# Optimization experiments

Hardware: AMD Instinct MI355X
Metric: run time of the kernel (lower is better)

The kernel has to match this reference:

```python
import jax, jax.numpy as jnp
import numpy as np

HIDDEN = 1024
H2 = HIDDEN // 2
LAYERS = 2
NUM_CONDS = 4


def _lstm_dir(x, Wih, Whh, b, reverse):
    # x: (B, T, I); Wih: (4*H2, I); Whh: (4*H2, H2); b: (4*H2,)
    B = x.shape[0]
    h2 = Whh.shape[1]
    pre = jnp.einsum('bti,gi->btg', x, Wih) + b  # precompute input contribution
    pre = jnp.swapaxes(pre, 0, 1)  # (T, B, 4*H2)
    if reverse:
        pre = pre[::-1]

    def step(carry, g_in):
        h, c = carry
        g = g_in + h @ Whh.T
        i, f, gg, o = jnp.split(g, 4, axis=-1)
        c = jax.nn.sigmoid(f) * c + jax.nn.sigmoid(i) * jnp.tanh(gg)
        h = jax.nn.sigmoid(o) * jnp.tanh(c)
        return (h, c), h

    init = (jnp.zeros((B, h2), x.dtype), jnp.zeros((B, h2), x.dtype))
    _, hs = jax.lax.scan(step, init, pre)
    if reverse:
        hs = hs[::-1]
    return jnp.swapaxes(hs, 0, 1)  # (B, T, H2)


def _bilstm(x, Wih, Whh, b):
    # Wih: (L, 2, 4*H2, I) — all layers share input width since embed_dim == hidden_dim
    out = x
    for l in range(Wih.shape[0]):
        fwd = _lstm_dir(out, Wih[l, 0], Whh[l, 0], b[l, 0], False)
        bwd = _lstm_dir(out, Wih[l, 1], Whh[l, 1], b[l, 1], True)
        out = jnp.concatenate([fwd, bwd], axis=-1)
    return out


def setup_inputs() -> dict:
    key = jax.random.key(0)
    ks = jax.random.split(key, 24)
    s = 0.02
    G = 4 * H2
    inp = {
        'question_embedding': jax.random.normal(ks[0], (32, 128, 1024), jnp.float32),
        'packed_column_embedding': jax.random.normal(ks[1], (640, 8, 1024), jnp.float32),
        'gold_num': jax.random.randint(ks[2], (32,), 0, 5),
        'gold_cols': jax.random.randint(ks[3], (32, 4), 0, 20),
        'gold_ops': jax.random.randint(ks[4], (32, 4), 0, 4),
        'num_columns': 20,
        'q_Wih': jax.random.normal(ks[5], (LAYERS, 2, G, 1024), jnp.float32) * s,
        'q_Whh': jax.random.normal(ks[6], (LAYERS, 2, G, H2), jnp.float32) * s,
        'q_b': jax.random.normal(ks[7], (LAYERS, 2, G), jnp.float32) * s,
        'c_Wih': jax.random.normal(ks[8], (LAYERS, 2, G, 1024), jnp.float32) * s,
        'c_Whh': jax.random.normal(ks[9], (LAYERS, 2, G, H2), jnp.float32) * s,
        'c_b': jax.random.normal(ks[10], (LAYERS, 2, G), jnp.float32) * s,
        'col_attn_w': jax.random.normal(ks[11], (1, HIDDEN), jnp.float32) * s,
        'col_attn_b': jnp.zeros((1,), jnp.float32),
        'ob_attn_W': jax.random.normal(ks[12], (HIDDEN, HIDDEN), jnp.float32) * s,
        'ob_attn_b': jnp.zeros((HIDDEN,), jnp.float32),
        'ob_col_W': jax.random.normal(ks[13], (HIDDEN, HIDDEN), jnp.float32) * s,
        'ob_col_b': jnp.zeros((HIDDEN,), jnp.float32),
        'q_proj_W': jax.random.normal(ks[14], (HIDDEN, HIDDEN), jnp.float32) * s,
        'q_proj_b': jnp.zeros((HIDDEN,), jnp.float32),
        'out1_W': jax.random.normal(ks[15], (HIDDEN, 3 * HIDDEN), jnp.float32) * s,
        'out1_b': jnp.zeros((HIDDEN,), jnp.float32),
        'out2_W': jax.random.normal(ks[16], (2, HIDDEN), jnp.float32) * s,
        'out2_b': jnp.zeros((2,), jnp.float32),
    }
    return inp


def _forward(question_embedding, packed_column_embedding, gold_num, gold_cols,
             num_columns, q_Wih, q_Whh, q_b, c_Wih, c_Whh, c_b,
             col_attn_w, col_attn_b, ob_attn_W, ob_attn_b, ob_col_W, ob_col_b,
             q_proj_W, q_proj_b, out1_W, out1_b, out2_W, out2_b):
    dt = question_embedding.dtype
    bs, Tq, _ = question_embedding.shape
    # compute_mask: nonzero token positions
    q_mask = (jnp.abs(question_embedding).sum(-1) != 0).astype(dt)  # (B, Tq)
    c_mask = (jnp.abs(packed_column_embedding).sum(-1) != 0).astype(dt)  # (P, Tc)

    q_enc = _bilstm(question_embedding, q_Wih, q_Whh, q_b)  # (B, Tq, H)
    c_enc = _bilstm(packed_column_embedding, c_Wih, c_Whh, c_b)  # (P, Tc, H)

    # attention-pool each column name: make_weight = masked softmax over tokens
    logits = jnp.einsum('pth,oh->pt', c_enc, col_attn_w) + col_attn_b[0]
    logits = jnp.where(c_mask > 0, logits, -jnp.inf)
    w = jax.nn.softmax(logits, axis=-1)
    col_pooled = jnp.einsum('pt,pth->ph', w, c_enc)  # (P, H)
    column_hidden = col_pooled.reshape(bs, num_columns, HIDDEN)  # (B, NC, H)

    # get_observed_column_hidden (torch.no_grad): gather gold columns, zero-pad
    K = gold_cols.shape[1]
    gn = jnp.minimum(gold_num, K)
    cond_mask = (jnp.arange(K)[None, :] < gn[:, None]).astype(dt)  # (B, K)
    observed = jnp.take_along_axis(column_hidden, gold_cols[:, :, None], axis=1)  # (B, K, H)
    observed = observed * cond_mask[..., None]
    observed = jax.lax.stop_gradient(observed)
    cond_mask = jax.lax.stop_gradient(cond_mask)

    # mm_attention over question tokens
    att_key = observed @ ob_attn_W.T + ob_attn_b  # (B, K, H)
    scores = jnp.einsum('bkh,bqh->bkq', att_key, q_enc)
    scores = jnp.where(q_mask[:, None, :] > 0, scores, -jnp.inf)
    attn = jax.nn.softmax(scores, axis=-1)
    q_hidden = jnp.einsum('bkq,bqh->bkh', attn, q_enc)  # (B, K, H)

    vec = jnp.concatenate([observed @ ob_col_W.T + ob_col_b,
                           q_hidden @ q_proj_W.T + q_proj_b], axis=-1)  # (B, K, 2H)
    # broadcast concat: (B, K, Tq, 3H)
    x = jnp.concatenate([
        jnp.broadcast_to(q_enc[:, None], (bs, K, Tq, HIDDEN)),
        jnp.broadcast_to(vec[:, :, None], (bs, K, Tq, 2 * HIDDEN)),
    ], axis=-1)
    h1 = jnp.tanh(x @ out1_W.T + out1_b)
    pos = h1 @ out2_W.T + out2_b  # (B, K, Tq, 2)

    full_mask = cond_mask[:, :, None] * q_mask[:, None, :]  # (B, K, Tq)
    pos = jnp.where(full_mask[..., None] > 0, pos, -jnp.inf)
    return pos[..., 0], pos[..., 1]


def reference(question_embedding, packed_column_embedding, gold_num, gold_cols,
              gold_ops, num_columns, q_Wih, q_Whh, q_b, c_Wih, c_Whh, c_b,
              col_attn_w, col_attn_b, ob_attn_W, ob_attn_b, ob_col_W, ob_col_b,
              q_proj_W, q_proj_b, out1_W, out1_b, out2_W, out2_b):
    # gold_ops is accepted but unused by the original forward
    return _forward(question_embedding, packed_column_embedding, gold_num, gold_cols,
                    num_columns, q_Wih, q_Whh, q_b, c_Wih, c_Whh, c_b,
                    col_attn_w, col_attn_b, ob_attn_W, ob_attn_b, ob_col_W, ob_col_b,
                    q_proj_W, q_proj_b, out1_W, out1_b, out2_W, out2_b)
```

## Files before the change

kernel.cpp:

```cpp
#include <hip/hip_runtime.h>
#include <math.h>


using f32x4 = __attribute__((ext_vector_type(4))) float;
using s16x8 = __attribute__((ext_vector_type(8))) short;
typedef unsigned long long ulong_t;

#define ASYNC_COPY16(gsrc, ldst)                                               \
  __builtin_amdgcn_global_load_lds(                                            \
      (const __attribute__((address_space(1))) void*)(gsrc),                   \
      (__attribute__((address_space(3))) void*)(ldst), 16, 0, 0)

#define LSBM 0x0001000100010001ull

static __device__ __forceinline__ float sigm(float x) {
  return __builtin_amdgcn_rcpf(1.0f + __expf(-x));
}
static __device__ __forceinline__ float tanh_f(float x) {
  return 1.0f - 2.0f * __builtin_amdgcn_rcpf(__expf(2.0f * x) + 1.0f);
}

static __device__ __forceinline__ unsigned short f2b_one(float x) {
  unsigned int u = __float_as_uint(x);
  u = (u + 0x7FFFu + ((u >> 16) & 1u)) >> 16;
  return (unsigned short)u;
}

__global__ __launch_bounds__(256) void f2b_kernel(
    const float* __restrict__ in, unsigned short* __restrict__ out, int n4)
{
  const int i = blockIdx.x * 256 + threadIdx.x;
  if (i >= n4) return;
  const float4 v = ((const float4*)in)[i];
  ushort4 r;
  r.x = f2b_one(v.x); r.y = f2b_one(v.y);
  r.z = f2b_one(v.z); r.w = f2b_one(v.w);
  ((ushort4*)out)[i] = r;
}

__global__ __launch_bounds__(256) void mask_kernel(
    const float* __restrict__ qe, const float* __restrict__ pce,
    float* __restrict__ qmask, float* __restrict__ cmask)
{
  const int w = threadIdx.x >> 6;
  const int lane = threadIdx.x & 63;
  const int row = blockIdx.x * 4 + w;
  const float* src = (row < 4096) ? (qe + (size_t)row * 1024)
                                  : (pce + (size_t)(row - 4096) * 1024);
  float s = 0.f;
#pragma unroll
  for (int j = 0; j < 16; ++j) s += fabsf(src[lane + j * 64]);
#pragma unroll
  for (int off = 32; off > 0; off >>= 1) s += __shfl_down(s, off, 64);
  if (lane == 0) {
    const float m = (s != 0.f) ? 1.f : 0.f;
    if (row < 4096) qmask[row] = m;
    else cmask[row - 4096] = m;
  }
}

__global__ __launch_bounds__(256) void mfma_gemm_kernel(
    const unsigned short* __restrict__ X, const unsigned short* __restrict__ W,
    const float* __restrict__ bias, float* __restrict__ C,
    int K, int ldx, int ldw, int k0w, int ldc, int c0)
{
  __shared__ unsigned short As[128 * 32];
  __shared__ unsigned short Bs[128 * 32];
  const int tid = threadIdx.x;
  const int w = tid >> 6;
  const int l = tid & 63;
  const int m0 = blockIdx.y * 128;
  const int n0 = blockIdx.x * 128;
  const int wm = (w >> 1) * 64;
  const int wn = (w & 1) * 64;

  const unsigned short* xg =
      X + (size_t)(m0 + w * 32 + (l >> 2)) * ldx + (l & 3) * 8;
  const unsigned short* wgp =
      W + (size_t)(n0 + w * 32 + (l >> 2)) * ldw + k0w + (l & 3) * 8;
  unsigned short* asb = As + w * 1024;
  unsigned short* bsb = Bs + w * 1024;

  const int fr = l & 15;
  const int fq = l >> 4;
  const unsigned short* aRd = As + (wm + fr) * 32 + fq * 8;
  const unsigned short* bRd = Bs + (wn + fr) * 32 + fq * 8;

  f32x4 acc[4][4];
#pragma unroll
  for (int i = 0; i < 4; ++i)
#pragma unroll
    for (int j = 0; j < 4; ++j) acc[i][j] = (f32x4){0.f, 0.f, 0.f, 0.f};

  for (int k0 = 0; k0 < K; k0 += 32) {
    ASYNC_COPY16(xg + k0, asb);
    ASYNC_COPY16(xg + (size_t)16 * ldx + k0, asb + 512);
    ASYNC_COPY16(wgp + k0, bsb);
    ASYNC_COPY16(wgp + (size_t)16 * ldw + k0, bsb + 512);
    __syncthreads();
    s16x8 a[4], b[4];
#pragma unroll
    for (int i = 0; i < 4; ++i) a[i] = *(const s16x8*)(aRd + i * 512);
#pragma unroll
    for (int j = 0; j < 4; ++j) b[j] = *(const s16x8*)(bRd + j * 512);
#pragma unroll
    for (int i = 0; i < 4; ++i)
#pragma unroll
      for (int j = 0; j < 4; ++j)
        acc[i][j] = __builtin_amdgcn_mfma_f32_16x16x32_bf16(
            a[i], b[j], acc[i][j], 0, 0, 0);
    __syncthreads();
  }

#pragma unroll
  for (int j = 0; j < 4; ++j) {
    const int col = n0 + wn + j * 16 + fr;
    const float bj = bias ? bias[col] : 0.f;
#pragma unroll
    for (int i = 0; i < 4; ++i) {
      const int row = m0 + wm + i * 16 + fq * 4;
#pragma unroll
      for (int r = 0; r < 4; ++r)
        C[(size_t)(row + r) * ldc + c0 + col] = acc[i][j][r] + bj;
    }
  }
}

__global__ __launch_bounds__(256) void gemm_kernel(
    const float* __restrict__ X, const float* __restrict__ W,
    const float* __restrict__ bias, float* __restrict__ C,
    int M, int N, int K, int ldx, int ldw, int k0w, int ldc, int c0)
{
  __shared__ float Xs[16][68];
  __shared__ float Ws[16][68];
  const int tid = threadIdx.x;
  const int m0 = blockIdx.y * 64;
  const int n0 = blockIdx.x * 64;
  const int lrow = tid >> 2;
  const int lkk = (tid & 3) << 2;
  const float* Xp = X + (size_t)(m0 + lrow) * ldx + lkk;
  const float* Wp = W + (size_t)(n0 + lrow) * ldw + k0w + lkk;
  const int tm = (tid >> 4) << 2;
  const int tn = (tid & 15) << 2;
  float acc[4][4];
#pragma unroll
  for (int i = 0; i < 4; ++i)
#pragma unroll
    for (int j = 0; j < 4; ++j) acc[i][j] = 0.f;

  for (int k0 = 0; k0 < K; k0 += 16) {
    const float4 xv = *(const float4*)(Xp + k0);
    const float4 wv = *(const float4*)(Wp + k0);
    Xs[lkk + 0][lrow] = xv.x; Xs[lkk + 1][lrow] = xv.y;
    Xs[lkk + 2][lrow] = xv.z; Xs[lkk + 3][lrow] = xv.w;
    Ws[lkk + 0][lrow] = wv.x; Ws[lkk + 1][lrow] = wv.y;
    Ws[lkk + 2][lrow] = wv.z; Ws[lkk + 3][lrow] = wv.w;
    __syncthreads();
#pragma unroll
    for (int kk = 0; kk < 16; ++kk) {
      const float4 a4 = *(const float4*)&Xs[kk][tm];
      const float4 b4 = *(const float4*)&Ws[kk][tn];
      const float av[4] = {a4.x, a4.y, a4.z, a4.w};
      const float bv[4] = {b4.x, b4.y, b4.z, b4.w};
#pragma unroll
      for (int i = 0; i < 4; ++i)
#pragma unroll
        for (int j = 0; j < 4; ++j) acc[i][j] += av[i] * bv[j];
    }
    __syncthreads();
  }
  float bvv[4] = {0.f, 0.f, 0.f, 0.f};
  if (bias) {
#pragma unroll
    for (int j = 0; j < 4; ++j) bvv[j] = bias[n0 + tn + j];
  }
#pragma unroll
  for (int i = 0; i < 4; ++i)
#pragma unroll
    for (int j = 0; j < 4; ++j)
      C[(size_t)(m0 + tm + i) * ldc + c0 + n0 + tn + j] = acc[i][j] + bvv[j];
}

template <int NT>
__global__ __launch_bounds__(512, 2) void lstm_seq_kernel(
    const float* __restrict__ pre,
    const unsigned short* __restrict__ whh,
    unsigned short* __restrict__ hbuf,
    float* __restrict__ out,
    int T, unsigned* __restrict__ bar, unsigned base)
{
  __shared__ float preS[NT][4][16][34];
  __shared__ float Tr[8][4][4][20];
  __shared__ unsigned short hS[NT * 16][36];
  __shared__ unsigned short hR[NT * 16][528];
  const int tid = threadIdx.x;
  const int v = tid >> 6;
  const int l = tid & 63;
  const int d = blockIdx.x >> 4;
  const int w = blockIdx.x & 15;
  const int bg = blockIdx.y;
  const int fr = l & 15;
  const int fq = l >> 4;
  const int ubase = w * 32;
  const int unit = ubase + v * 4 + fq;
  const int nbase = bg * (NT * 16);
  const size_t SLOT = (size_t)640 * 512;
  unsigned* ctr = bar + (d * 8 + bg) * 16;
  unsigned short* sl = hbuf + (size_t)d * 3 * SLOT;

  s16x8 afr[16];
  {
    const unsigned short* arow = whh + (size_t)d * 2048 * 512 +
        ((size_t)(fr >> 2) * 512 + ubase + v * 4 + (fr & 3)) * 512 + fq * 8;
#pragma unroll
    for (int kk = 0; kk < 16; ++kk)
      afr[kk] = *(const s16x8*)(arow + kk * 32);
  }

  float creg[NT];
#pragma unroll
  for (int i = 0; i < NT; ++i) creg[i] = 0.f;

  const int sc = tid & 7;
  const int sn = (tid >> 3) & 15;
  const int sg = tid >> 7;

  for (int s = 0; s < 3; ++s) {
    ulong_t* cb = (ulong_t*)(sl + (size_t)s * SLOT + (size_t)nbase * 512 + ubase);
    for (int i = tid; i < NT * 16 * 8; i += 512)
      __hip_atomic_store(cb + (size_t)(i >> 3) * 128 + (i & 7), LSBM,
                         __ATOMIC_RELAXED, __HIP_MEMORY_SCOPE_AGENT);
  }
  {
    const int tt0 = d ? (T - 1) : 0;
#pragma unroll
    for (int nt = 0; nt < NT; ++nt) {
      const int n = nbase + nt * 16 + sn;
      const float4 pv = *(const float4*)(
          pre + ((size_t)n * T + tt0) * 4096 + d * 2048 + sg * 512 + ubase +
          sc * 4);
      *(float4*)&preS[nt][sg][sn][sc * 4] = pv;
    }
  }
  __syncthreads();
  if (tid == 0) {
    __hip_atomic_fetch_add(ctr, 1u, __ATOMIC_RELAXED,
                           __HIP_MEMORY_SCOPE_AGENT);
    const unsigned target = base + 16u;
    long spins = 0;
    while (__hip_atomic_load(ctr, __ATOMIC_RELAXED,
                             __HIP_MEMORY_SCOPE_AGENT) < target) {
      __builtin_amdgcn_s_sleep(1);
      if (++spins > 2000000L) break;
    }
  }
  __syncthreads();

  float hnreg[NT];
  for (int t = 0; t < T; ++t) {
    const int tt = d ? (T - 1 - t) : t;
    const unsigned wtag = (unsigned)((t / 3) & 1);
    unsigned short* wr = sl + (size_t)(t % 3) * SLOT;

    if (t > 0) {
      const unsigned rtag = (unsigned)(((t - 1) / 3) & 1);
      const ulong_t want = rtag ? LSBM : 0ull;
      const ulong_t* hq =
          (const ulong_t*)(sl + (size_t)((t + 2) % 3) * SLOT) +
          (size_t)nbase * 128;
      ulong_t u[4 * NT];
      bool ok = false;
      int it = 0;
      while (!ok && it < 200000) {
#pragma unroll
        for (int i = 0; i < 2 * NT; ++i) {
          const int cid = i * 512 + tid;
          const ulong_t* p = hq + (size_t)(cid >> 6) * 128 + (cid & 63) * 2;
          u[2 * i] = __hip_atomic_load(p, __ATOMIC_RELAXED,
                                       __HIP_MEMORY_SCOPE_AGENT);
          u[2 * i + 1] = __hip_atomic_load(p + 1, __ATOMIC_RELAXED,
                                           __HIP_MEMORY_SCOPE_AGENT);
        }
        bool bad = false;
#pragma unroll
        for (int i = 0; i < 4 * NT; ++i) bad |= ((u[i] & LSBM) != want);
        ok = !bad;
        ++it;
        if (!ok && it > 12) __builtin_amdgcn_s_sleep(1);
      }
#pragma unroll
      for (int i = 0; i < 2 * NT; ++i) {
        const int cid = i * 512 + tid;
        ulong_t* dst = (ulong_t*)&hR[cid >> 6][(cid & 63) * 8];
        dst[0] = u[2 * i];
        dst[1] = u[2 * i + 1];
      }
    }
    float4 pv[NT];
    if (t + 1 < T) {
      const int ttn = d ? (T - 2 - t) : (t + 1);
#pragma unroll
      for (int nt = 0; nt < NT; ++nt) {
        const int n = nbase + nt * 16 + sn;
        pv[nt] = *(const float4*)(
            pre + ((size_t)n * T + ttn) * 4096 + d * 2048 + sg * 512 + ubase +
            sc * 4);
      }
    }
    asm volatile("s_waitcnt lgkmcnt(0)" ::: "memory");
    __builtin_amdgcn_s_barrier();
    __builtin_amdgcn_sched_barrier(0);

#pragma unroll
    for (int nt = 0; nt < NT; ++nt) {
      f32x4 acc = (f32x4){0.f, 0.f, 0.f, 0.f};
      if (t > 0) {
        const unsigned short* bRd = &hR[nt * 16 + fr][fq * 8];
#pragma unroll
        for (int kk = 0; kk < 16; ++kk) {
          const s16x8 bv = *(const s16x8*)(bRd + kk * 32);
          acc = __builtin_amdgcn_mfma_f32_16x16x32_bf16(afr[kk], bv, acc,
                                                        0, 0, 0);
        }
      }
#pragma unroll
      for (int r = 0; r < 4; ++r) Tr[v][fq][r][fr] = acc[r];
      const int uu = v * 4 + fq;
      const float gi = Tr[v][0][fq][fr] + preS[nt][0][fr][uu];
      const float gf = Tr[v][1][fq][fr] + preS[nt][1][fr][uu];
      const float gg = Tr[v][2][fq][fr] + preS[nt][2][fr][uu];
      const float go = Tr[v][3][fq][fr] + preS[nt][3][fr][uu];
      const float cn = sigm(gf) * creg[nt] + sigm(gi) * tanh_f(gg);
      const float hn = sigm(go) * tanh_f(cn);
      creg[nt] = cn;
      hnreg[nt] = hn;
      hS[nt * 16 + fr][uu] =
          (unsigned short)((f2b_one(hn) & 0xFFFEu) | wtag);
      const int n0i = nbase + nt * 16 + fr;
      (void)n0i;
    }
    asm volatile("s_waitcnt lgkmcnt(0)" ::: "memory");
    __builtin_amdgcn_s_barrier();
    __builtin_amdgcn_sched_barrier(0);

    if (t + 1 < T) {
#pragma unroll
      for (int nt = 0; nt < NT; ++nt)
        *(float4*)&preS[nt][sg][sn][sc * 4] = pv[nt];
    }
    {
      const int un = tid & 7;
      const int nl = tid >> 3;
      for (int p = nl; p < NT * 16; p += 64) {
        const ulong_t val = *(const ulong_t*)&hS[p][un * 4];
        __hip_atomic_store(
            (ulong_t*)(wr + (size_t)(nbase + p) * 512 + ubase) + un, val,
            __ATOMIC_RELAXED, __HIP_MEMORY_SCOPE_AGENT);
      }
    }
#pragma unroll
    for (int nt = 0; nt < NT; ++nt) {
      const int n = nbase + nt * 16 + fr;
      out[((size_t)n * T + tt) * 1024 + d * 512 + unit] = hnreg[nt];
    }
  }
}

__global__ __launch_bounds__(256) void colpool_kernel(
    const float* __restrict__ cenc, const float* __restrict__ caw,
    const float* __restrict__ cab, const float* __restrict__ cmask,
    float* __restrict__ colh)
{
  __shared__ float part[8][33];
  __shared__ float wbuf[8];
  const int p = blockIdx.x;
  const int t = threadIdx.x >> 5;
  const int ln = threadIdx.x & 31;
  const float* row = cenc + ((size_t)p * 8 + t) * 1024;
  float s = 0.f;
  for (int j = ln; j < 1024; j += 32) s += row[j] * caw[j];
  part[t][ln] = s;
  __syncthreads();
  if (threadIdx.x < 8) {
    float lg = 0.f;
    for (int i = 0; i < 32; ++i) lg += part[threadIdx.x][i];
    lg += cab[0];
    wbuf[threadIdx.x] = (cmask[p * 8 + threadIdx.x] > 0.f) ? lg : -INFINITY;
  }
  __syncthreads();
  if (threadIdx.x == 0) {
    float mx = -INFINITY;
    for (int i = 0; i < 8; ++i) mx = fmaxf(mx, wbuf[i]);
    float e[8];
    float sum = 0.f;
    for (int i = 0; i < 8; ++i) { e[i] = expf(wbuf[i] - mx); sum += e[i]; }
    for (int i = 0; i < 8; ++i) wbuf[i] = e[i] / sum;
  }
  __syncthreads();
  for (int h = threadIdx.x; h < 1024; h += 256) {
    float a = 0.f;
#pragma unroll
    for (int i = 0; i < 8; ++i) a += wbuf[i] * cenc[((size_t)p * 8 + i) * 1024 + h];
    colh[(size_t)p * 1024 + h] = a;
  }
}

__global__ __launch_bounds__(256) void gather_kernel(
    const float* __restrict__ colh, const int* __restrict__ gold_num,
    const int* __restrict__ gold_cols, const int* __restrict__ ncol,
    float* __restrict__ obs)
{
  const int idx = blockIdx.x * 256 + threadIdx.x;
  const int h = idx & 1023;
  const int k = (idx >> 10) & 3;
  const int b = idx >> 12;
  int gn = gold_num[b];
  if (gn > 4) gn = 4;
  const float m = (k < gn) ? 1.f : 0.f;
  const int col = gold_cols[b * 4 + k];
  const int NC = ncol[0];
  obs[idx] = m * colh[(size_t)(b * NC + col) * 1024 + h];
}

__global__ __launch_bounds__(128) void attn_kernel(
    const float* __restrict__ akey, const float* __restrict__ qenc,
    const float* __restrict__ qmask, float* __restrict__ qhid)
{
  __shared__ float ak[1024];
  __shared__ float red[128];
  __shared__ float at[128];
  const int bk = blockIdx.x;
  const int b = bk >> 2;
  const int tid = threadIdx.x;
  for (int i = tid; i < 1024; i += 128) ak[i] = akey[(size_t)bk * 1024 + i];
  __syncthreads();
  const float* qrow = qenc + ((size_t)b * 128 + tid) * 1024;
  float s = 0.f;
  for (int hh = 0; hh < 1024; hh += 4) {
    const float4 qv = *(const float4*)(qrow + hh);
    s += ak[hh] * qv.x + ak[hh + 1] * qv.y + ak[hh + 2] * qv.z + ak[hh + 3] * qv.w;
  }
  s = (qmask[b * 128 + tid] > 0.f) ? s : -INFINITY;
  at[tid] = s;
  red[tid] = s;
  __syncthreads();
  for (int off = 64; off > 0; off >>= 1) {
    if (tid < off) red[tid] = fmaxf(red[tid], red[tid + off]);
    __syncthreads();
  }
  const float mx = red[0];
  __syncthreads();
  const float e = expf(at[tid] - mx);
  red[tid] = e;
  __syncthreads();
  for (int off = 64; off > 0; off >>= 1) {
    if (tid < off) red[tid] += red[tid + off];
    __syncthreads();
  }
  const float inv = 1.f / red[0];
  __syncthreads();
  at[tid] = e * inv;
  __syncthreads();
  for (int h = tid; h < 1024; h += 128) {
    float a = 0.f;
    for (int q = 0; q < 128; ++q)
      a += at[q] * qenc[((size_t)b * 128 + q) * 1024 + h];
    qhid[(size_t)bk * 1024 + h] = a;
  }
}

__global__ __launch_bounds__(64) void final_kernel(
    const float* __restrict__ A, const float* __restrict__ Bm,
    const float* __restrict__ w2, const float* __restrict__ b2,
    const int* __restrict__ gold_num, const float* __restrict__ qmask,
    float* __restrict__ out)
{
  const int bkq = blockIdx.x;
  const int q = bkq & 127;
  const int k = (bkq >> 7) & 3;
  const int b = bkq >> 9;
  int gn = gold_num[b];
  if (gn > 4) gn = 4;
  const bool act = (k < gn) && (qmask[b * 128 + q] > 0.f);
  const int lane = threadIdx.x;
  const int obase = (b * 4 + k) * 128 + q;
  if (!act) {
    if (lane == 0) {
      out[obase] = -1e30f;
      out[16384 + obase] = -1e30f;
    }
    return;
  }
  const float* Ar = A + ((size_t)b * 128 + q) * 1024;
  const float* Br = Bm + (size_t)(b * 4 + k) * 1024;
  float s0 = 0.f, s1 = 0.f;
  for (int o = lane; o < 1024; o += 64) {
    const float v = tanhf(Ar[o] + Br[o]);
    s0 += v * w2[o];
    s1 += v * w2[1024 + o];
  }
#pragma unroll
  for (int off = 32; off > 0; off >>= 1) {
    s0 += __shfl_down(s0, off, 64);
    s1 += __shfl_down(s1, off, 64);
  }
  if (lane == 0) {
    out[obase] = s0 + b2[0];
    out[16384 + obase] = s1 + b2[1];
  }
}

extern "C" void kernel_launch(void* const* d_in, const int* in_sizes, int n_in,
                              void* d_out, int out_size, void* d_ws, size_t ws_size,
                              hipStream_t stream)
{
  const float* qe      = (const float*)d_in[0];
  const float* pce     = (const float*)d_in[1];
  const int* gold_num  = (const int*)d_in[2];
  const int* gold_cols = (const int*)d_in[3];
  const int* ncol      = (const int*)d_in[5];
  const float* q_Wih   = (const float*)d_in[6];
  const float* q_Whh   = (const float*)d_in[7];
  const float* q_b     = (const float*)d_in[8];
  const float* c_Wih   = (const float*)d_in[9];
  const float* c_Whh   = (const float*)d_in[10];
  const float* c_b     = (const float*)d_in[11];
  const float* caw     = (const float*)d_in[12];
  const float* cab     = (const float*)d_in[13];
  const float* obaW    = (const float*)d_in[14];
  const float* obab    = (const float*)d_in[15];
  const float* obcW    = (const float*)d_in[16];
  const float* obcb    = (const float*)d_in[17];
  const float* qpW     = (const float*)d_in[18];
  const float* qpb     = (const float*)d_in[19];
  const float* o1W     = (const float*)d_in[20];
  const float* o1b     = (const float*)d_in[21];
  const float* o2W     = (const float*)d_in[22];
  const float* o2b     = (const float*)d_in[23];
  float* outp = (float*)d_out;

  float* ws = (float*)d_ws;
  size_t off = 0;
  float* pre  = ws + off; off += 640UL * 8 * 4096;
  float* bufA = ws + off; off += 640UL * 8 * 1024;
  float* bufB = ws + off; off += 640UL * 8 * 1024;
  float* colh = ws + off; off += 640UL * 1024;
  float* qmask = ws + off; off += 4096;
  float* cmask = ws + off; off += 5120;
  float* obs  = ws + off; off += 131072;
  float* akey = ws + off; off += 131072;
  float* qhid = ws + off; off += 131072;
  float* vec  = ws + off; off += 262144;
  float* Bm   = ws + off; off += 131072;
  unsigned short* xb = (unsigned short*)(ws + off); off += 2621440;
  unsigned short* wb = (unsigned short*)(ws + off); off += 2097152;
  unsigned short* whhq = (unsigned short*)(ws + off); off += 2097152;
  unsigned short* whhc = (unsigned short*)(ws + off); off += 2097152;
  unsigned short* hbuf = (unsigned short*)(ws + off); off += 983040;
  unsigned* bar = (unsigned*)(ws + off); off += 256;
  float* Amat = pre;

  const dim3 blk(256);
  auto cvt = [&](const float* src, unsigned short* dst, int n) {
    hipLaunchKernelGGL(f2b_kernel, dim3((n / 4 + 255) / 256), blk, 0, stream,
                       src, dst, n / 4);
  };

  hipMemsetAsync(bar, 0, 1024, stream);

  hipLaunchKernelGGL(mask_kernel, dim3(2304), blk, 0, stream, qe, pce, qmask, cmask);

  cvt(q_Whh, whhq, 4194304);
  cvt(c_Whh, whhc, 4194304);

  for (int l = 0; l < 2; ++l) {
    const float* xin = (l == 0) ? pce : bufA;
    float* enc = (l == 0) ? bufA : bufB;
    cvt(xin, xb, 5242880);
    cvt(c_Wih + (size_t)l * 4194304, wb, 4194304);
    hipLaunchKernelGGL(mfma_gemm_kernel, dim3(4096 / 128, 5120 / 128), blk, 0,
                       stream, xb, wb, c_b + l * 4096, pre,
                       1024, 1024, 1024, 0, 4096, 0);
    hipLaunchKernelGGL((lstm_seq_kernel<5>), dim3(32, 8), dim3(512), 0, stream,
                       pre, whhc + (size_t)l * 2 * 2048 * 512, hbuf, enc,
                       8, bar, (unsigned)(l * 16));
  }
  hipLaunchKernelGGL(colpool_kernel, dim3(640), blk, 0, stream,
                     bufB, caw, cab, cmask, colh);
  hipLaunchKernelGGL(gather_kernel, dim3(512), blk, 0, stream,
                     colh, gold_num, gold_cols, ncol, obs);

  for (int l = 0; l < 2; ++l) {
    const float* xin = (l == 0) ? qe : bufA;
    float* enc = (l == 0) ? bufA : bufB;
    cvt(xin, xb, 4194304);
    cvt(q_Wih + (size_t)l * 4194304, wb, 4194304);
    hipLaunchKernelGGL(mfma_gemm_kernel, dim3(4096 / 128, 4096 / 128), blk, 0,
                       stream, xb, wb, q_b + l * 4096, pre,
                       1024, 1024, 1024, 0, 4096, 0);
    hipLaunchKernelGGL((lstm_seq_kernel<2>), dim3(32, 1), dim3(512), 0, stream,
                       pre, whhq + (size_t)l * 2 * 2048 * 512, hbuf, enc,
                       128, bar, (unsigned)(32 + l * 16));
  }
  const float* qenc = bufB;

  hipLaunchKernelGGL(gemm_kernel, dim3(16, 2), blk, 0, stream,
                     obs, obaW, obab, akey, 128, 1024, 1024, 1024, 1024, 0, 1024, 0);
  hipLaunchKernelGGL(attn_kernel, dim3(128), dim3(128), 0, stream,
                     akey, qenc, qmask, qhid);
  hipLaunchKernelGGL(gemm_kernel, dim3(16, 2), blk, 0, stream,
                     obs, obcW, obcb, vec, 128, 1024, 1024, 1024, 1024, 0, 2048, 0);
  hipLaunchKernelGGL(gemm_kernel, dim3(16, 2), blk, 0, stream,
                     qhid, qpW, qpb, vec, 128, 1024, 1024, 1024, 1024, 0, 2048, 1024);
  cvt(qenc, xb, 4194304);
  cvt(o1W, wb, 3145728);
  hipLaunchKernelGGL(mfma_gemm_kernel, dim3(1024 / 128, 4096 / 128), blk, 0,
                     stream, xb, wb, o1b, Amat, 1024, 1024, 3072, 0, 1024, 0);
  hipLaunchKernelGGL(gemm_kernel, dim3(16, 2), blk, 0, stream,
                     vec, o1W, nullptr, Bm, 128, 1024, 2048, 2048, 3072, 1024, 1024, 0);
  hipLaunchKernelGGL(final_kernel, dim3(16384), dim3(64), 0, stream,
                     Amat, Bm, o2W, o2b, gold_num, qmask, outp);
}
```

Before: 1.976 ms.

## Publish LSTM hidden state directly from registers and prefetch peer state speculatively

The recurrent LSTM kernel no longer stages new hidden values in shared memory before storing them. Lanes pair bf16 values with a shuffle and write 32-bit atomic stores straight to the global exchange buffer, and the output store moves inline. After the barrier, each block speculatively loads the next step's peer hidden state and re-polls only if the tag bits are stale, aiming to take the spin-wait load latency off the critical path. Smaller edits drop the occupancy hint from launch bounds, shorten the spin before sleeping, and swap in fast exp/tanh in the auxiliary kernels. The cost is more scattered small global stores and a possible wasted prefetch when peers lag.

Measured after the change: 1.969 ms. Within noise of the previous version (-0.4%).

```diff
diff --git a/kernel.cpp b/kernel.cpp
--- a/kernel.cpp
+++ b/kernel.cpp
@@ -182,7 +182,7 @@
 }
 
 template <int NT>
-__global__ __launch_bounds__(512, 2) void lstm_seq_kernel(
+__global__ __launch_bounds__(512) void lstm_seq_kernel(
     const float* __restrict__ pre,
     const unsigned short* __restrict__ whh,
     unsigned short* __restrict__ hbuf,
@@ -191,7 +191,6 @@
 {
   __shared__ float preS[NT][4][16][34];
   __shared__ float Tr[8][4][4][20];
-  __shared__ unsigned short hS[NT * 16][36];
   __shared__ unsigned short hR[NT * 16][528];
   const int tid = threadIdx.x;
   const int v = tid >> 6;
@@ -256,7 +255,7 @@
   }
   __syncthreads();
 
-  float hnreg[NT];
+  ulong_t u[4 * NT];
   for (int t = 0; t < T; ++t) {
     const int tt = d ? (T - 1 - t) : t;
     const unsigned wtag = (unsigned)((t / 3) & 1);
@@ -268,25 +267,29 @@
       const ulong_t* hq =
           (const ulong_t*)(sl + (size_t)((t + 2) % 3) * SLOT) +
           (size_t)nbase * 128;
-      ulong_t u[4 * NT];
-      bool ok = false;
-      int it = 0;
-      while (!ok && it < 200000) {
-#pragma unroll
-        for (int i = 0; i < 2 * NT; ++i) {
-          const int cid = i * 512 + tid;
-          const ulong_t* p = hq + (size_t)(cid >> 6) * 128 + (cid & 63) * 2;
-          u[2 * i] = __hip_atomic_load(p, __ATOMIC_RELAXED,
-                                       __HIP_MEMORY_SCOPE_AGENT);
-          u[2 * i + 1] = __hip_atomic_load(p + 1, __ATOMIC_RELAXED,
-                                           __HIP_MEMORY_SCOPE_AGENT);
+      bool bad0 = false;
+#pragma unroll
+      for (int i = 0; i < 4 * NT; ++i) bad0 |= ((u[i] & LSBM) != want);
+      if (bad0) {
+        bool ok = false;
+        int it = 0;
+        while (!ok && it < 200000) {
+#pragma unroll
+          for (int i = 0; i < 2 * NT; ++i) {
+            const int cid = i * 512 + tid;
+            const ulong_t* p = hq + (size_t)(cid >> 6) * 128 + (cid & 63) * 2;
+            u[2 * i] = __hip_atomic_load(p, __ATOMIC_RELAXED,
+                                         __HIP_MEMORY_SCOPE_AGENT);
+            u[2 * i + 1] = __hip_atomic_load(p + 1, __ATOMIC_RELAXED,
+                                             __HIP_MEMORY_SCOPE_AGENT);
+          }
+          bool bad = false;
+#pragma unroll
+          for (int i = 0; i < 4 * NT; ++i) bad |= ((u[i] & LSBM) != want);
+          ok = !bad;
+          ++it;
+          if (!ok && it > 8) __builtin_amdgcn_s_sleep(1);
         }
-        bool bad = false;
-#pragma unroll
-        for (int i = 0; i < 4 * NT; ++i) bad |= ((u[i] & LSBM) != want);
-        ok = !bad;
-        ++it;
-        if (!ok && it > 12) __builtin_amdgcn_s_sleep(1);
       }
 #pragma unroll
       for (int i = 0; i < 2 * NT; ++i) {
@@ -333,11 +336,17 @@
       const float cn = sigm(gf) * creg[nt] + sigm(gi) * tanh_f(gg);
       const float hn = sigm(go) * tanh_f(cn);
       creg[nt] = cn;
-      hnreg[nt] = hn;
-      hS[nt * 16 + fr][uu] =
-          (unsigned short)((f2b_one(hn) & 0xFFFEu) | wtag);
-      const int n0i = nbase + nt * 16 + fr;
-      (void)n0i;
+      const unsigned hv =
+          (unsigned)((f2b_one(hn) & 0xFFFEu) | wtag);
+      const unsigned pv16 = (unsigned)__shfl_xor((int)hv, 16, 64);
+      const int n = nbase + nt * 16 + fr;
+      if ((fq & 1) == 0) {
+        const unsigned pk = hv | (pv16 << 16);
+        __hip_atomic_store(
+            (unsigned*)(wr + (size_t)n * 512) + (unit >> 1), pk,
+            __ATOMIC_RELAXED, __HIP_MEMORY_SCOPE_AGENT);
+      }
+      out[((size_t)n * T + tt) * 1024 + d * 512 + unit] = hn;
     }
     asm volatile("s_waitcnt lgkmcnt(0)" ::: "memory");
     __builtin_amdgcn_s_barrier();
@@ -347,21 +356,18 @@
 #pragma unroll
       for (int nt = 0; nt < NT; ++nt)
         *(float4*)&preS[nt][sg][sn][sc * 4] = pv[nt];
-    }
-    {
-      const int un = tid & 7;
-      const int nl = tid >> 3;
-      for (int p = nl; p < NT * 16; p += 64) {
-        const ulong_t val = *(const ulong_t*)&hS[p][un * 4];
-        __hip_atomic_store(
-            (ulong_t*)(wr + (size_t)(nbase + p) * 512 + ubase) + un, val,
-            __ATOMIC_RELAXED, __HIP_MEMORY_SCOPE_AGENT);
+      const ulong_t* hq =
+          (const ulong_t*)(sl + (size_t)((t + 3) % 3) * SLOT) +
+          (size_t)nbase * 128;
+#pragma unroll
+      for (int i = 0; i < 2 * NT; ++i) {
+        const int cid = i * 512 + tid;
+        const ulong_t* p = hq + (size_t)(cid >> 6) * 128 + (cid & 63) * 2;
+        u[2 * i] = __hip_atomic_load(p, __ATOMIC_RELAXED,
+                                     __HIP_MEMORY_SCOPE_AGENT);
+        u[2 * i + 1] = __hip_atomic_load(p + 1, __ATOMIC_RELAXED,
+                                         __HIP_MEMORY_SCOPE_AGENT);
       }
-    }
-#pragma unroll
-    for (int nt = 0; nt < NT; ++nt) {
-      const int n = nbase + nt * 16 + fr;
-      out[((size_t)n * T + tt) * 1024 + d * 512 + unit] = hnreg[nt];
     }
   }
 }
@@ -393,7 +399,7 @@
     for (int i = 0; i < 8; ++i) mx = fmaxf(mx, wbuf[i]);
     float e[8];
     float sum = 0.f;
-    for (int i = 0; i < 8; ++i) { e[i] = expf(wbuf[i] - mx); sum += e[i]; }
+    for (int i = 0; i < 8; ++i) { e[i] = __expf(wbuf[i] - mx); sum += e[i]; }
     for (int i = 0; i < 8; ++i) wbuf[i] = e[i] / sum;
   }
   __syncthreads();
@@ -450,7 +456,7 @@
   }
   const float mx = red[0];
   __syncthreads();
-  const float e = expf(at[tid] - mx);
+  const float e = __expf(at[tid] - mx);
   red[tid] = e;
   __syncthreads();
   for (int off = 64; off > 0; off >>= 1) {
@@ -495,7 +501,7 @@
   const float* Br = Bm + (size_t)(b * 4 + k) * 1024;
   float s0 = 0.f, s1 = 0.f;
   for (int o = lane; o < 1024; o += 64) {
-    const float v = tanhf(Ar[o] + Br[o]);
+    const float v = tanh_f(Ar[o] + Br[o]);
     s0 += v * w2[o];
     s1 += v * w2[1024 + o];
   }
```
